# Performance work log

Measured on AMD Instinct MI355X. Metric: run time of the kernel, lower is better.

Reference implementation:

```python
import jax, jax.numpy as jnp
import numpy as np

N, E = 50000, 1600000
F_IN, C1, H, C2, G, NCLS = 256, 16, 4, 32, 64, 10


def setup_inputs() -> dict:
    ks = jax.random.split(jax.random.key(0), 14)
    x = jax.random.normal(ks[0], (N, F_IN), dtype=jnp.float32)
    edge_index = jax.random.randint(ks[1], (2, E), 0, N, dtype=jnp.int32)
    batch = jnp.sort(jax.random.randint(ks[2], (N,), 0, G, dtype=jnp.int32))
    s1 = 1.0 / np.sqrt(F_IN)
    s2 = 1.0 / np.sqrt(H * C1)
    s3 = 1.0 / np.sqrt(C2)
    return {
        "x": x,
        "edge_index": edge_index,
        "batch": batch,
        "W1": jax.random.normal(ks[3], (F_IN, H * C1), jnp.float32) * s1,
        "att_src1": jax.random.normal(ks[4], (H, C1), jnp.float32) * s2,
        "att_dst1": jax.random.normal(ks[5], (H, C1), jnp.float32) * s2,
        "b1": jnp.zeros((H * C1,), jnp.float32),
        "W2": jax.random.normal(ks[6], (H * C1, C2), jnp.float32) * s2,
        "att_src2": jax.random.normal(ks[7], (1, C2), jnp.float32) * s3,
        "att_dst2": jax.random.normal(ks[8], (1, C2), jnp.float32) * s3,
        "b2": jnp.zeros((C2,), jnp.float32),
        "fc_w": jax.random.normal(ks[9], (C2, NCLS), jnp.float32) * s3,
        "fc_b": jnp.zeros((NCLS,), jnp.float32),
    }


def _gat_conv(x, src, dst, W, a_src, a_dst, b, concat):
    # PyG GATConv: linear per head, LeakyReLU(0.2) edge scores,
    # softmax over incoming edges per destination node, weighted scatter-sum.
    n = x.shape[0]
    heads, ch = a_src.shape
    h = (x @ W).reshape(n, heads, ch)                       # [N, H, C]
    a_s = (h * a_src).sum(-1)                               # [N, H]
    a_d = (h * a_dst).sum(-1)                               # [N, H]
    e = jax.nn.leaky_relu(a_s[src] + a_d[dst], 0.2)         # [E', H]
    m = jax.ops.segment_max(e, dst, num_segments=n)         # [N, H]
    w = jnp.exp(e - m[dst])
    den = jax.ops.segment_sum(w, dst, num_segments=n)
    alpha = w / den[dst]                                    # [E', H]
    out = jax.ops.segment_sum(alpha[:, :, None] * h[src], dst, num_segments=n)
    out = out.reshape(n, heads * ch) if concat else out.mean(axis=1)
    return out + b


def reference(x, edge_index, batch, W1, att_src1, att_dst1, b1,
              W2, att_src2, att_dst2, b2, fc_w, fc_b):
    n = x.shape[0]
    loops = jnp.arange(n, dtype=edge_index.dtype)           # add_self_loops=True
    src = jnp.concatenate([edge_index[0], loops])
    dst = jnp.concatenate([edge_index[1], loops])

    h = jax.nn.elu(_gat_conv(x, src, dst, W1, att_src1, att_dst1, b1, True))
    h = jax.nn.elu(_gat_conv(h, src, dst, W2, att_src2, att_dst2, b2, False))

    # global mean pool over graphs
    sums = jax.ops.segment_sum(h, batch, num_segments=G)    # [G, C2]
    cnt = jax.ops.segment_sum(jnp.ones((n,), h.dtype), batch, num_segments=G)
    pooled = sums / jnp.maximum(cnt, 1.0)[:, None]

    logits = pooled @ fc_w + fc_b
    return jax.nn.log_softmax(logits, axis=1)
```

## Files before the change

### kernel.cpp

```cpp
#include <hip/hip_runtime.h>
#include <hip/hip_bf16.h>

#define GV 64
#define NCLSV 10
#define C2V 32
#define CHUNK 256

using short8 = __attribute__((ext_vector_type(8))) short;
using short4v = __attribute__((ext_vector_type(4))) short;
using f32x4 = __attribute__((ext_vector_type(4))) float;

__device__ __forceinline__ float lrelu(float v) { return v > 0.f ? v : 0.2f * v; }
__device__ __forceinline__ float eluf(float v) { return v > 0.f ? v : expf(v) - 1.f; }

__device__ __forceinline__ unsigned short fbf(float f) {
    unsigned u = __float_as_uint(f);
    u += 0x7fff + ((u >> 16) & 1);
    return (unsigned short)(u >> 16);
}
__device__ __forceinline__ float bff(unsigned short h) {
    return __uint_as_float((unsigned)h << 16);
}

__global__ void zero_kernel(int* p, int n) {
    int i = blockIdx.x * blockDim.x + threadIdx.x;
    if (i < n) p[i] = 0;
}

__global__ void wprep_kernel(const float* __restrict__ W1, const float* __restrict__ W2,
                             short* __restrict__ wt, short* __restrict__ wt2) {
    int t = blockIdx.x * blockDim.x + threadIdx.x;
    for (int e = t; e < 16384; e += gridDim.x * blockDim.x) {
        int k = e >> 6, ch = e & 63;
        wt[ch * 256 + k] = (short)fbf(W1[e]);
    }
    for (int e = t; e < 2048; e += gridDim.x * blockDim.x) {
        int k = e >> 5, ch = e & 31;
        wt2[ch * 64 + k] = (short)fbf(W2[e]);
    }
}

__global__ __launch_bounds__(256) void gemm1_mfma_kernel(
    const float* __restrict__ x, const short* __restrict__ wt,
    const float* __restrict__ as_w, const float* __restrict__ ad_w,
    unsigned short* __restrict__ h1lo, unsigned short* __restrict__ h1hi,
    float* __restrict__ as1, float* __restrict__ ad1, int N) {
    __shared__ __align__(16) short xs[32 * 256];
    int b0 = blockIdx.x * 32;
    int tid = threadIdx.x;
    #pragma unroll
    for (int i = 0; i < 8; ++i) {
        int e = (tid + i * 256) * 4;
        int node = e >> 8, k = e & 255;
        float4 v = make_float4(0.f, 0.f, 0.f, 0.f);
        if (b0 + node < N) v = *(const float4*)&x[(size_t)(b0 + node) * 256 + k];
        short4v hv;
        hv[0] = (short)fbf(v.x); hv[1] = (short)fbf(v.y);
        hv[2] = (short)fbf(v.z); hv[3] = (short)fbf(v.w);
        int bo = node * 512 + k * 2;
        int sw = bo ^ ((node & 7) << 4);
        *(short4v*)((char*)xs + sw) = hv;
    }
    __syncthreads();
    int w = tid >> 6, lane = tid & 63;
    int ng = w >> 1, cg = w & 1;
    int g = lane >> 4, q = lane & 15;
    int rowb = ng * 16 + q;
    int kb = g * 8;
    f32x4 acc[2];
    acc[0] = (f32x4){0.f, 0.f, 0.f, 0.f};
    acc[1] = (f32x4){0.f, 0.f, 0.f, 0.f};
    #pragma unroll
    for (int ks = 0; ks < 8; ++ks) {
        int kk = ks * 32 + kb;
        int off = (rowb * 512 + kk * 2) ^ ((rowb & 7) << 4);
        short8 a = *(const short8*)((const char*)xs + off);
        #pragma unroll
        for (int ct = 0; ct < 2; ++ct) {
            int ch = cg * 32 + ct * 16 + q;
            short8 b = *(const short8*)(wt + ch * 256 + kk);
            acc[ct] = __builtin_amdgcn_mfma_f32_16x16x32_bf16(a, b, acc[ct], 0, 0, 0);
        }
    }
    unsigned short* dst = cg ? h1hi : h1lo;
    #pragma unroll
    for (int ct = 0; ct < 2; ++ct) {
        int chi = cg * 32 + ct * 16 + q;
        int ch32 = ct * 16 + q;
        float asw = as_w[chi], adw = ad_w[chi];
        int head = cg * 2 + ct;
        #pragma unroll
        for (int r = 0; r < 4; ++r) {
            int node = b0 + ng * 16 + g * 4 + r;
            float val = acc[ct][r];
            if (node < N) dst[(size_t)node * 32 + ch32] = fbf(val);
            float vs = val * asw, vd = val * adw;
            vs += __shfl_xor(vs, 1); vs += __shfl_xor(vs, 2);
            vs += __shfl_xor(vs, 4); vs += __shfl_xor(vs, 8);
            vd += __shfl_xor(vd, 1); vd += __shfl_xor(vd, 2);
            vd += __shfl_xor(vd, 4); vd += __shfl_xor(vd, 8);
            if (q == 0 && node < N) {
                as1[node * 4 + head] = vs;
                ad1[node * 4 + head] = vd;
            }
        }
    }
}

__global__ __launch_bounds__(256) void bucketPre_kernel(
    const int* __restrict__ ei, int E, int EE, int* __restrict__ bcnt,
    int* __restrict__ pbase) {
    __shared__ int hist[256];
    int span = (EE + gridDim.x - 1) / gridDim.x;
    int s0 = blockIdx.x * span;
    int s1 = min(s0 + span, EE);
    hist[threadIdx.x] = 0;
    __syncthreads();
    for (int i = s0 + threadIdx.x; i < s1; i += 256) {
        int d = (i < E) ? ei[E + i] : i - E;
        atomicAdd(&hist[d >> 8], 1);
    }
    __syncthreads();
    int c = hist[threadIdx.x];
    int base = 0;
    if (c) base = atomicAdd(&bcnt[threadIdx.x], c);
    pbase[blockIdx.x * 256 + threadIdx.x] = base;
}

__global__ void bscan_kernel(const int* __restrict__ bcnt, int* __restrict__ bucketoff,
                             int* __restrict__ rowoff, int N, int EE) {
    __shared__ int wtot[4];
    int v = bcnt[threadIdx.x];
    int lane = threadIdx.x & 63, w = threadIdx.x >> 6;
    int inc = v;
    for (int o = 1; o < 64; o <<= 1) { int t = __shfl_up(inc, o); if (lane >= o) inc += t; }
    if (lane == 63) wtot[w] = inc;
    __syncthreads();
    int woff = 0;
    #pragma unroll
    for (int i = 0; i < 4; ++i) woff += (i < w) ? wtot[i] : 0;
    bucketoff[threadIdx.x + 1] = woff + inc;
    if (threadIdx.x == 0) { bucketoff[0] = 0; rowoff[N] = EE; }
}

__global__ __launch_bounds__(256) void bucketA_kernel(
    const int* __restrict__ ei, int E, int EE,
    const int* __restrict__ bucketoff, const int* __restrict__ pbase,
    int* __restrict__ bbuf) {
    __shared__ int base[256];
    __shared__ int cur[256];
    int span = (EE + gridDim.x - 1) / gridDim.x;
    int s0 = blockIdx.x * span;
    int s1 = min(s0 + span, EE);
    if (s0 >= s1) return;
    base[threadIdx.x] = bucketoff[threadIdx.x] + pbase[blockIdx.x * 256 + threadIdx.x];
    cur[threadIdx.x] = 0;
    __syncthreads();
    for (int i = s0 + threadIdx.x; i < s1; i += 256) {
        int s, d;
        if (i < E) { s = ei[i]; d = ei[E + i]; } else { s = d = i - E; }
        int b = d >> 8;
        int lr = atomicAdd(&cur[b], 1);
        bbuf[base[b] + lr] = ((d & 255) << 24) | s;
    }
}

__global__ __launch_bounds__(256) void bucketB_kernel(
    const int* __restrict__ bucketoff, const int* __restrict__ bbuf,
    int* __restrict__ rowoff, int* __restrict__ ssrc, int N) {
    int k = blockIdx.x;
    __shared__ int cnt[256];
    __shared__ int excl[256];
    __shared__ int cur[256];
    __shared__ int wtot[4];
    cnt[threadIdx.x] = 0; cur[threadIdx.x] = 0;
    __syncthreads();
    int lo = bucketoff[k], hi = bucketoff[k + 1];
    for (int i = lo + threadIdx.x; i < hi; i += 256)
        atomicAdd(&cnt[(bbuf[i] >> 24) & 255], 1);
    __syncthreads();
    int v = cnt[threadIdx.x];
    int lane = threadIdx.x & 63, w = threadIdx.x >> 6;
    int inc = v;
    for (int o = 1; o < 64; o <<= 1) { int t = __shfl_up(inc, o); if (lane >= o) inc += t; }
    if (lane == 63) wtot[w] = inc;
    __syncthreads();
    int woff = 0;
    #pragma unroll
    for (int i = 0; i < 4; ++i) woff += (i < w) ? wtot[i] : 0;
    int e = woff + inc - v;
    excl[threadIdx.x] = e;
    int dst = (k << 8) + threadIdx.x;
    if (dst < N) rowoff[dst] = lo + e;
    __syncthreads();
    for (int i = lo + threadIdx.x; i < hi; i += 256) {
        int pv = bbuf[i];
        int dlow = (pv >> 24) & 255;
        int lr = atomicAdd(&cur[dlow], 1);
        ssrc[lo + excl[dlow] + lr] = pv & 0xFFFFFF;
    }
}

__global__ __launch_bounds__(256) void gat1_kernel(
    const int* __restrict__ rowoff, const int* __restrict__ ssrc,
    const float* __restrict__ as1, const float* __restrict__ ad1,
    const unsigned short* __restrict__ tab, const float* __restrict__ b1,
    unsigned short* __restrict__ h2b, int N, int ho) {
    __shared__ int s_s[4][CHUNK];
    __shared__ float s_w[4][2 * CHUNK];
    int wv = threadIdx.x >> 6;
    int lane = threadIdx.x & 63;
    int row = blockIdx.x * 4 + wv;
    if (row >= N) return;
    int beg = rowoff[row], end = rowoff[row + 1];
    int hp = lane >> 5, j = lane & 31;
    int par = lane >> 2, co = lane & 3;
    int hq = co >> 1;
    float adv = ad1[row * 4 + ho + hp];
    float den = 0.f;
    float a[8];
    #pragma unroll
    for (int i = 0; i < 8; ++i) a[i] = 0.f;
    int* sb = s_s[wv];
    float* wb = s_w[wv];
    for (int cb = beg; cb < end; cb += CHUNK) {
        int clen = min(end - cb, CHUNK);
        for (int t = j; t < clen; t += 32) {
            int s = ssrc[cb + t];
            if (hp == 0) sb[t] = s;
            float w = __expf(lrelu(as1[s * 4 + ho + hp] + adv));
            wb[t * 2 + hp] = w;
            den += w;
        }
        for (int t = par; t < clen; t += 16) {
            int s0 = sb[t];
            float w0 = wb[t * 2 + hq];
            short8 p = *(const short8*)&tab[(size_t)s0 * 32 + 8 * co];
            a[0] += w0 * bff((unsigned short)p[0]);
            a[1] += w0 * bff((unsigned short)p[1]);
            a[2] += w0 * bff((unsigned short)p[2]);
            a[3] += w0 * bff((unsigned short)p[3]);
            a[4] += w0 * bff((unsigned short)p[4]);
            a[5] += w0 * bff((unsigned short)p[5]);
            a[6] += w0 * bff((unsigned short)p[6]);
            a[7] += w0 * bff((unsigned short)p[7]);
        }
    }
    den += __shfl_xor(den, 1);
    den += __shfl_xor(den, 2);
    den += __shfl_xor(den, 4);
    den += __shfl_xor(den, 8);
    den += __shfl_xor(den, 16);
    float dd = __shfl(den, hq << 5);
    #pragma unroll
    for (int i = 0; i < 8; ++i) {
        a[i] += __shfl_xor(a[i], 4);
        a[i] += __shfl_xor(a[i], 8);
        a[i] += __shfl_xor(a[i], 16);
        a[i] += __shfl_xor(a[i], 32);
    }
    if (par == 0) {
        float r = 1.f / dd;
        int cbase = (ho >> 1) * 32 + 8 * co;
        short8 o;
        #pragma unroll
        for (int i = 0; i < 8; ++i)
            o[i] = (short)fbf(eluf(a[i] * r + b1[cbase + i]));
        *(short8*)&h2b[(size_t)row * 64 + cbase] = o;
    }
}

__global__ __launch_bounds__(256) void gemm2_mfma_kernel(
    const unsigned short* __restrict__ h2b, const short* __restrict__ wt2,
    const float* __restrict__ as_w, const float* __restrict__ ad_w,
    unsigned short* __restrict__ t2b, float* __restrict__ as2, float* __restrict__ ad2, int N) {
    __shared__ __align__(16) short xs[64 * 64];
    int b0 = blockIdx.x * 64;
    int tid = threadIdx.x;
    #pragma unroll
    for (int i = 0; i < 2; ++i) {
        int e = (tid + i * 256) * 8;
        int node = e >> 6, k = e & 63;
        short8 v = (short8){0, 0, 0, 0, 0, 0, 0, 0};
        if (b0 + node < N) v = *(const short8*)&h2b[(size_t)(b0 + node) * 64 + k];
        int bo = node * 128 + k * 2;
        int sw = bo ^ ((node & 7) << 4);
        *(short8*)((char*)xs + sw) = v;
    }
    __syncthreads();
    int w = tid >> 6, lane = tid & 63;
    int g = lane >> 4, q = lane & 15;
    int rowb = w * 16 + q;
    int kb = g * 8;
    f32x4 acc[2];
    acc[0] = (f32x4){0.f, 0.f, 0.f, 0.f};
    acc[1] = (f32x4){0.f, 0.f, 0.f, 0.f};
    #pragma unroll
    for (int ks = 0; ks < 2; ++ks) {
        int kk = ks * 32 + kb;
        int off = (rowb * 128 + kk * 2) ^ ((rowb & 7) << 4);
        short8 a = *(const short8*)((const char*)xs + off);
        #pragma unroll
        for (int ct = 0; ct < 2; ++ct) {
            int ch = ct * 16 + q;
            short8 b = *(const short8*)(wt2 + ch * 64 + kk);
            acc[ct] = __builtin_amdgcn_mfma_f32_16x16x32_bf16(a, b, acc[ct], 0, 0, 0);
        }
    }
    float asw0 = as_w[q], adw0 = ad_w[q];
    float asw1 = as_w[16 + q], adw1 = ad_w[16 + q];
    #pragma unroll
    for (int r = 0; r < 4; ++r) {
        int node = b0 + w * 16 + g * 4 + r;
        float v0 = acc[0][r], v1 = acc[1][r];
        if (node < N) {
            t2b[(size_t)node * 32 + q] = fbf(v0);
            t2b[(size_t)node * 32 + 16 + q] = fbf(v1);
        }
        float vs = v0 * asw0 + v1 * asw1;
        float vd = v0 * adw0 + v1 * adw1;
        vs += __shfl_xor(vs, 1); vs += __shfl_xor(vs, 2);
        vs += __shfl_xor(vs, 4); vs += __shfl_xor(vs, 8);
        vd += __shfl_xor(vd, 1); vd += __shfl_xor(vd, 2);
        vd += __shfl_xor(vd, 4); vd += __shfl_xor(vd, 8);
        if (q == 0 && node < N) {
            as2[node] = vs;
            ad2[node] = vd;
        }
    }
}

__global__ __launch_bounds__(256) void gat2_kernel(
    const int* __restrict__ rowoff, const int* __restrict__ ssrc,
    const float* __restrict__ as2, const float* __restrict__ ad2,
    const unsigned short* __restrict__ t2b, const float* __restrict__ b2,
    float* __restrict__ h3, int N) {
    __shared__ int s_s[4][CHUNK];
    __shared__ float s_w[4][CHUNK];
    int wv = threadIdx.x >> 6;
    int lane = threadIdx.x & 63;
    int row = blockIdx.x * 4 + wv;
    if (row >= N) return;
    int beg = rowoff[row], end = rowoff[row + 1];
    int par = lane >> 2, co = lane & 3;
    float adv = ad2[row];
    float den = 0.f;
    float a[8];
    #pragma unroll
    for (int i = 0; i < 8; ++i) a[i] = 0.f;
    int* sb = s_s[wv];
    float* wb = s_w[wv];
    for (int cb = beg; cb < end; cb += CHUNK) {
        int clen = min(end - cb, CHUNK);
        for (int t = lane; t < clen; t += 64) {
            int s = ssrc[cb + t];
            sb[t] = s;
            float w = __expf(lrelu(as2[s] + adv));
            wb[t] = w;
            den += w;
        }
        for (int t = par; t < clen; t += 16) {
            int s0 = sb[t];
            float w0 = wb[t];
            short8 p = *(const short8*)&t2b[(size_t)s0 * 32 + 8 * co];
            a[0] += w0 * bff((unsigned short)p[0]);
            a[1] += w0 * bff((unsigned short)p[1]);
            a[2] += w0 * bff((unsigned short)p[2]);
            a[3] += w0 * bff((unsigned short)p[3]);
            a[4] += w0 * bff((unsigned short)p[4]);
            a[5] += w0 * bff((unsigned short)p[5]);
            a[6] += w0 * bff((unsigned short)p[6]);
            a[7] += w0 * bff((unsigned short)p[7]);
        }
    }
    den += __shfl_xor(den, 1);
    den += __shfl_xor(den, 2);
    den += __shfl_xor(den, 4);
    den += __shfl_xor(den, 8);
    den += __shfl_xor(den, 16);
    den += __shfl_xor(den, 32);
    #pragma unroll
    for (int i = 0; i < 8; ++i) {
        a[i] += __shfl_xor(a[i], 4);
        a[i] += __shfl_xor(a[i], 8);
        a[i] += __shfl_xor(a[i], 16);
        a[i] += __shfl_xor(a[i], 32);
    }
    if (par == 0) {
        float r = 1.f / den;
        float4 o0, o1;
        o0.x = eluf(a[0] * r + b2[8 * co]);
        o0.y = eluf(a[1] * r + b2[8 * co + 1]);
        o0.z = eluf(a[2] * r + b2[8 * co + 2]);
        o0.w = eluf(a[3] * r + b2[8 * co + 3]);
        o1.x = eluf(a[4] * r + b2[8 * co + 4]);
        o1.y = eluf(a[5] * r + b2[8 * co + 5]);
        o1.z = eluf(a[6] * r + b2[8 * co + 6]);
        o1.w = eluf(a[7] * r + b2[8 * co + 7]);
        *(float4*)&h3[(size_t)row * 32 + 8 * co] = o0;
        *(float4*)&h3[(size_t)row * 32 + 8 * co + 4] = o1;
    }
}

__device__ __forceinline__ int lowerb(const int* __restrict__ a, int n, int v) {
    int lo = 0, hi = n;
    while (lo < hi) {
        int mid = (lo + hi) >> 1;
        if (a[mid] < v) lo = mid + 1; else hi = mid;
    }
    return lo;
}

__global__ __launch_bounds__(256) void pool_kernel(
    const float* __restrict__ h3, const int* __restrict__ batch,
    float* __restrict__ pooled, float* __restrict__ cnt, int N) {
    int g = blockIdx.x;
    __shared__ int bounds[2];
    if (threadIdx.x == 0) bounds[0] = lowerb(batch, N, g);
    else if (threadIdx.x == 1) bounds[1] = lowerb(batch, N, g + 1);
    __syncthreads();
    int lo = bounds[0], hi = bounds[1];
    int c = threadIdx.x & 31;
    int grp = threadIdx.x >> 5;
    float s = 0.f;
    for (int n = lo + grp; n < hi; n += 8) s += h3[(size_t)n * 32 + c];
    __shared__ float red[8][33];
    red[grp][c] = s;
    __syncthreads();
    if (grp == 0) {
        float t = 0.f;
        for (int k = 0; k < 8; ++k) t += red[k][c];
        pooled[g * C2V + c] = t;
        if (c == 0) cnt[g] = (float)(hi - lo);
    }
}

__global__ void final_kernel(const float* __restrict__ pooled, const float* __restrict__ cnt,
                             const float* __restrict__ fc_w, const float* __restrict__ fc_b,
                             float* __restrict__ out) {
    int g = threadIdx.x;
    if (g >= GV) return;
    float c = cnt[g];
    c = c > 1.f ? c : 1.f;
    float p[C2V];
    for (int j = 0; j < C2V; ++j) p[j] = pooled[g * C2V + j] / c;
    float l[NCLSV];
    float mx = -1e30f;
    for (int k = 0; k < NCLSV; ++k) {
        float acc = fc_b[k];
        for (int j = 0; j < C2V; ++j) acc += p[j] * fc_w[j * NCLSV + k];
        l[k] = acc;
        mx = fmaxf(mx, acc);
    }
    float s = 0.f;
    for (int k = 0; k < NCLSV; ++k) s += expf(l[k] - mx);
    float lse = mx + logf(s);
    for (int k = 0; k < NCLSV; ++k) out[g * NCLSV + k] = l[k] - lse;
}

extern "C" void kernel_launch(void* const* d_in, const int* in_sizes, int n_in,
                              void* d_out, int out_size, void* d_ws, size_t ws_size,
                              hipStream_t stream) {
    const float* x = (const float*)d_in[0];
    const int* ei = (const int*)d_in[1];
    const int* batch = (const int*)d_in[2];
    const float* W1 = (const float*)d_in[3];
    const float* att_src1 = (const float*)d_in[4];
    const float* att_dst1 = (const float*)d_in[5];
    const float* b1 = (const float*)d_in[6];
    const float* W2 = (const float*)d_in[7];
    const float* att_src2 = (const float*)d_in[8];
    const float* att_dst2 = (const float*)d_in[9];
    const float* b2 = (const float*)d_in[10];
    const float* fc_w = (const float*)d_in[11];
    const float* fc_b = (const float*)d_in[12];
    float* out = (float*)d_out;

    int N = in_sizes[0] / 256;
    int E = in_sizes[1] / 2;
    int EE = E + N;
    int NB = (N + 255) >> 8;

    float* ws = (float*)d_ws;
    size_t off = 0;
    int* bcnt = (int*)(ws + off);      off += 256;
    size_t zTot = off;
    int* pbase = (int*)(ws + off);     off += 1024 * 256;
    int* bucketoff = (int*)(ws + off); off += 257;
    float* pooled = ws + off;          off += (size_t)GV * C2V;
    float* cnt = ws + off;             off += (size_t)GV;
    int* rowoff = (int*)(ws + off);    off += (size_t)N + 1;
    int* bbuf = (int*)(ws + off);      off += (size_t)EE;
    int* ssrc = (int*)(ws + off);      off += (size_t)EE;
    short* wt = (short*)(ws + off);    off += 8192;
    short* wt2 = (short*)(ws + off);   off += 1024;
    unsigned short* h1lo = (unsigned short*)(ws + off); off += (size_t)16 * N;
    unsigned short* h1hi = (unsigned short*)(ws + off); off += (size_t)16 * N;
    float* as1 = ws + off;             off += (size_t)4 * N;
    float* ad1 = ws + off;             off += (size_t)4 * N;
    unsigned short* h2b = (unsigned short*)(ws + off); off += (size_t)32 * N;
    unsigned short* t2b = (unsigned short*)(ws + off); off += (size_t)16 * N;
    float* as2 = ws + off;             off += (size_t)N;
    float* ad2 = ws + off;             off += (size_t)N;
    float* h3 = ws + off;              off += (size_t)32 * N;

    zero_kernel<<<1, 256, 0, stream>>>((int*)ws, (int)zTot);
    wprep_kernel<<<9, 256, 0, stream>>>(W1, W2, wt, wt2);

    gemm1_mfma_kernel<<<(N + 31) / 32, 256, 0, stream>>>(
        x, wt, att_src1, att_dst1, h1lo, h1hi, as1, ad1, N);

    bucketPre_kernel<<<1024, 256, 0, stream>>>(ei, E, EE, bcnt, pbase);
    bscan_kernel<<<1, 256, 0, stream>>>(bcnt, bucketoff, rowoff, N, EE);
    bucketA_kernel<<<1024, 256, 0, stream>>>(ei, E, EE, bucketoff, pbase, bbuf);
    bucketB_kernel<<<NB, 256, 0, stream>>>(bucketoff, bbuf, rowoff, ssrc, N);

    gat1_kernel<<<(N + 3) / 4, 256, 0, stream>>>(rowoff, ssrc, as1, ad1, h1lo, b1, h2b, N, 0);
    gat1_kernel<<<(N + 3) / 4, 256, 0, stream>>>(rowoff, ssrc, as1, ad1, h1hi, b1, h2b, N, 2);

    gemm2_mfma_kernel<<<(N + 63) / 64, 256, 0, stream>>>(
        h2b, wt2, att_src2, att_dst2, t2b, as2, ad2, N);

    gat2_kernel<<<(N + 3) / 4, 256, 0, stream>>>(rowoff, ssrc, as2, ad2, t2b, b2, h3, N);

    pool_kernel<<<GV, 256, 0, stream>>>(h3, batch, pooled, cnt, N);
    final_kernel<<<1, 64, 0, stream>>>(pooled, cnt, fc_w, fc_b, out);
}
```

Before: 246.7 us.

## Precompute layer-1 edge weights in CSR build and merge GAT1 head passes

Moves computation of the layer-1 attention exponentials into the CSR bucket kernel, which writes a 16-byte record per edge holding the source index and four fp16 weights. The two per-head-pair gat1 launches become one kernel over a single 64-channel bf16 feature table, so edges are traversed once instead of twice and no shared-memory staging is needed. gat2 also drops its shared-memory chunk staging and computes weights inline per edge. This adds a 16B-per-edge write and read, and storing the weights in fp16 reduces their precision.

```diff
diff --git a/kernel.cpp b/kernel.cpp
--- a/kernel.cpp
+++ b/kernel.cpp
@@ -4,7 +4,6 @@
 #define GV 64
 #define NCLSV 10
 #define C2V 32
-#define CHUNK 256
 
 using short8 = __attribute__((ext_vector_type(8))) short;
 using short4v = __attribute__((ext_vector_type(4))) short;
@@ -20,6 +19,16 @@
 }
 __device__ __forceinline__ float bff(unsigned short h) {
     return __uint_as_float((unsigned)h << 16);
+}
+__device__ __forceinline__ unsigned f2h(float f) {
+    union { _Float16 h; unsigned short u; } cv;
+    cv.h = (_Float16)f;
+    return (unsigned)cv.u;
+}
+__device__ __forceinline__ float h2f(unsigned short u) {
+    union { unsigned short u; _Float16 h; } cv;
+    cv.u = u;
+    return (float)cv.h;
 }
 
 __global__ void zero_kernel(int* p, int n) {
@@ -43,8 +52,7 @@
 __global__ __launch_bounds__(256) void gemm1_mfma_kernel(
     const float* __restrict__ x, const short* __restrict__ wt,
     const float* __restrict__ as_w, const float* __restrict__ ad_w,
-    unsigned short* __restrict__ h1lo, unsigned short* __restrict__ h1hi,
-    float* __restrict__ as1, float* __restrict__ ad1, int N) {
+    unsigned short* __restrict__ h1b, float* __restrict__ as1, float* __restrict__ ad1, int N) {
     __shared__ __align__(16) short xs[32 * 256];
     int b0 = blockIdx.x * 32;
     int tid = threadIdx.x;
@@ -82,18 +90,16 @@
             acc[ct] = __builtin_amdgcn_mfma_f32_16x16x32_bf16(a, b, acc[ct], 0, 0, 0);
         }
     }
-    unsigned short* dst = cg ? h1hi : h1lo;
     #pragma unroll
     for (int ct = 0; ct < 2; ++ct) {
         int chi = cg * 32 + ct * 16 + q;
-        int ch32 = ct * 16 + q;
         float asw = as_w[chi], adw = ad_w[chi];
         int head = cg * 2 + ct;
         #pragma unroll
         for (int r = 0; r < 4; ++r) {
             int node = b0 + ng * 16 + g * 4 + r;
             float val = acc[ct][r];
-            if (node < N) dst[(size_t)node * 32 + ch32] = fbf(val);
+            if (node < N) h1b[(size_t)node * 64 + chi] = fbf(val);
             float vs = val * asw, vd = val * adw;
             vs += __shfl_xor(vs, 1); vs += __shfl_xor(vs, 2);
             vs += __shfl_xor(vs, 4); vs += __shfl_xor(vs, 8);
@@ -167,7 +173,8 @@
 
 __global__ __launch_bounds__(256) void bucketB_kernel(
     const int* __restrict__ bucketoff, const int* __restrict__ bbuf,
-    int* __restrict__ rowoff, int* __restrict__ ssrc, int N) {
+    const float* __restrict__ as1, const float* __restrict__ ad1,
+    int* __restrict__ rowoff, int* __restrict__ ssrc, int4* __restrict__ wrec, int N) {
     int k = blockIdx.x;
     __shared__ int cnt[256];
     __shared__ int excl[256];
@@ -193,80 +200,76 @@
     int dst = (k << 8) + threadIdx.x;
     if (dst < N) rowoff[dst] = lo + e;
     __syncthreads();
+    int dbase = k << 8;
     for (int i = lo + threadIdx.x; i < hi; i += 256) {
         int pv = bbuf[i];
         int dlow = (pv >> 24) & 255;
+        int s = pv & 0xFFFFFF;
+        int d = dbase + dlow;
         int lr = atomicAdd(&cur[dlow], 1);
-        ssrc[lo + excl[dlow] + lr] = pv & 0xFFFFFF;
+        int pos = lo + excl[dlow] + lr;
+        ssrc[pos] = s;
+        float4 a4 = *(const float4*)&as1[s * 4];
+        float4 d4 = *(const float4*)&ad1[d * 4];
+        float w0 = __expf(lrelu(a4.x + d4.x));
+        float w1 = __expf(lrelu(a4.y + d4.y));
+        float w2 = __expf(lrelu(a4.z + d4.z));
+        float w3 = __expf(lrelu(a4.w + d4.w));
+        int4 rec;
+        rec.x = s;
+        rec.y = (int)(f2h(w0) | (f2h(w1) << 16));
+        rec.z = (int)(f2h(w2) | (f2h(w3) << 16));
+        rec.w = 0;
+        wrec[pos] = rec;
     }
 }
 
 __global__ __launch_bounds__(256) void gat1_kernel(
-    const int* __restrict__ rowoff, const int* __restrict__ ssrc,
-    const float* __restrict__ as1, const float* __restrict__ ad1,
-    const unsigned short* __restrict__ tab, const float* __restrict__ b1,
-    unsigned short* __restrict__ h2b, int N, int ho) {
-    __shared__ int s_s[4][CHUNK];
-    __shared__ float s_w[4][2 * CHUNK];
+    const int* __restrict__ rowoff, const int4* __restrict__ wrec,
+    const unsigned short* __restrict__ h1b, const float* __restrict__ b1,
+    unsigned short* __restrict__ h2b, int N) {
     int wv = threadIdx.x >> 6;
     int lane = threadIdx.x & 63;
     int row = blockIdx.x * 4 + wv;
     if (row >= N) return;
     int beg = rowoff[row], end = rowoff[row + 1];
-    int hp = lane >> 5, j = lane & 31;
-    int par = lane >> 2, co = lane & 3;
-    int hq = co >> 1;
-    float adv = ad1[row * 4 + ho + hp];
+    int par = lane >> 3, co = lane & 7, hq = co >> 1;
     float den = 0.f;
     float a[8];
     #pragma unroll
     for (int i = 0; i < 8; ++i) a[i] = 0.f;
-    int* sb = s_s[wv];
-    float* wb = s_w[wv];
-    for (int cb = beg; cb < end; cb += CHUNK) {
-        int clen = min(end - cb, CHUNK);
-        for (int t = j; t < clen; t += 32) {
-            int s = ssrc[cb + t];
-            if (hp == 0) sb[t] = s;
-            float w = __expf(lrelu(as1[s * 4 + ho + hp] + adv));
-            wb[t * 2 + hp] = w;
-            den += w;
-        }
-        for (int t = par; t < clen; t += 16) {
-            int s0 = sb[t];
-            float w0 = wb[t * 2 + hq];
-            short8 p = *(const short8*)&tab[(size_t)s0 * 32 + 8 * co];
-            a[0] += w0 * bff((unsigned short)p[0]);
-            a[1] += w0 * bff((unsigned short)p[1]);
-            a[2] += w0 * bff((unsigned short)p[2]);
-            a[3] += w0 * bff((unsigned short)p[3]);
-            a[4] += w0 * bff((unsigned short)p[4]);
-            a[5] += w0 * bff((unsigned short)p[5]);
-            a[6] += w0 * bff((unsigned short)p[6]);
-            a[7] += w0 * bff((unsigned short)p[7]);
-        }
-    }
-    den += __shfl_xor(den, 1);
-    den += __shfl_xor(den, 2);
-    den += __shfl_xor(den, 4);
+    for (int t = beg + par; t < end; t += 8) {
+        int4 rec = wrec[t];
+        unsigned wpair = (hq & 2) ? (unsigned)rec.z : (unsigned)rec.y;
+        unsigned wb = (hq & 1) ? (wpair >> 16) : (wpair & 0xFFFFu);
+        float w = h2f((unsigned short)wb);
+        den += w;
+        short8 p = *(const short8*)&h1b[(size_t)rec.x * 64 + 8 * co];
+        a[0] += w * bff((unsigned short)p[0]);
+        a[1] += w * bff((unsigned short)p[1]);
+        a[2] += w * bff((unsigned short)p[2]);
+        a[3] += w * bff((unsigned short)p[3]);
+        a[4] += w * bff((unsigned short)p[4]);
+        a[5] += w * bff((unsigned short)p[5]);
+        a[6] += w * bff((unsigned short)p[6]);
+        a[7] += w * bff((unsigned short)p[7]);
+    }
     den += __shfl_xor(den, 8);
     den += __shfl_xor(den, 16);
-    float dd = __shfl(den, hq << 5);
+    den += __shfl_xor(den, 32);
     #pragma unroll
     for (int i = 0; i < 8; ++i) {
-        a[i] += __shfl_xor(a[i], 4);
         a[i] += __shfl_xor(a[i], 8);
         a[i] += __shfl_xor(a[i], 16);
         a[i] += __shfl_xor(a[i], 32);
     }
     if (par == 0) {
-        float r = 1.f / dd;
-        int cbase = (ho >> 1) * 32 + 8 * co;
+        float r = 1.f / den;
         short8 o;
         #pragma unroll
         for (int i = 0; i < 8; ++i)
-            o[i] = (short)fbf(eluf(a[i] * r + b1[cbase + i]));
-        *(short8*)&h2b[(size_t)row * 64 + cbase] = o;
+            o[i] = (short)fbf(eluf(a[i] * r + b1[8 * co + i]));
+        *(short8*)&h2b[(size_t)row * 64 + 8 * co] = o;
     }
 }
 
@@ -335,8 +338,6 @@
     const float* __restrict__ as2, const float* __restrict__ ad2,
     const unsigned short* __restrict__ t2b, const float* __restrict__ b2,
     float* __restrict__ h3, int N) {
-    __shared__ int s_s[4][CHUNK];
-    __shared__ float s_w[4][CHUNK];
     int wv = threadIdx.x >> 6;
     int lane = threadIdx.x & 63;
     int row = blockIdx.x * 4 + wv;
@@ -348,33 +349,20 @@
     float a[8];
     #pragma unroll
     for (int i = 0; i < 8; ++i) a[i] = 0.f;
-    int* sb = s_s[wv];
-    float* wb = s_w[wv];
-    for (int cb = beg; cb < end; cb += CHUNK) {
-        int clen = min(end - cb, CHUNK);
-        for (int t = lane; t < clen; t += 64) {
-            int s = ssrc[cb + t];
-            sb[t] = s;
-            float w = __expf(lrelu(as2[s] + adv));
-            wb[t] = w;
-            den += w;
-        }
-        for (int t = par; t < clen; t += 16) {
-            int s0 = sb[t];
-            float w0 = wb[t];
-            short8 p = *(const short8*)&t2b[(size_t)s0 * 32 + 8 * co];
-            a[0] += w0 * bff((unsigned short)p[0]);
-            a[1] += w0 * bff((unsigned short)p[1]);
-            a[2] += w0 * bff((unsigned short)p[2]);
-            a[3] += w0 * bff((unsigned short)p[3]);
-            a[4] += w0 * bff((unsigned short)p[4]);
-            a[5] += w0 * bff((unsigned short)p[5]);
-            a[6] += w0 * bff((unsigned short)p[6]);
-            a[7] += w0 * bff((unsigned short)p[7]);
-        }
-    }
-    den += __shfl_xor(den, 1);
-    den += __shfl_xor(den, 2);
+    for (int t = beg + par; t < end; t += 16) {
+        int s0 = ssrc[t];
+        float w = __expf(lrelu(as2[s0] + adv));
+        den += w;
+        short8 p = *(const short8*)&t2b[(size_t)s0 * 32 + 8 * co];
+        a[0] += w * bff((unsigned short)p[0]);
+        a[1] += w * bff((unsigned short)p[1]);
+        a[2] += w * bff((unsigned short)p[2]);
+        a[3] += w * bff((unsigned short)p[3]);
+        a[4] += w * bff((unsigned short)p[4]);
+        a[5] += w * bff((unsigned short)p[5]);
+        a[6] += w * bff((unsigned short)p[6]);
+        a[7] += w * bff((unsigned short)p[7]);
+    }
     den += __shfl_xor(den, 4);
     den += __shfl_xor(den, 8);
     den += __shfl_xor(den, 16);
@@ -492,10 +480,11 @@
     int* rowoff = (int*)(ws + off);    off += (size_t)N + 1;
     int* bbuf = (int*)(ws + off);      off += (size_t)EE;
     int* ssrc = (int*)(ws + off);      off += (size_t)EE;
+    off = (off + 3) & ~(size_t)3;
+    int4* wrec = (int4*)(ws + off);    off += (size_t)4 * EE;
     short* wt = (short*)(ws + off);    off += 8192;
     short* wt2 = (short*)(ws + off);   off += 1024;
-    unsigned short* h1lo = (unsigned short*)(ws + off); off += (size_t)16 * N;
-    unsigned short* h1hi = (unsigned short*)(ws + off); off += (size_t)16 * N;
+    unsigned short* h1b = (unsigned short*)(ws + off); off += (size_t)32 * N;
     float* as1 = ws + off;             off += (size_t)4 * N;
     float* ad1 = ws + off;             off += (size_t)4 * N;
     unsigned short* h2b = (unsigned short*)(ws + off); off += (size_t)32 * N;
@@ -508,15 +497,14 @@
     wprep_kernel<<<9, 256, 0, stream>>>(W1, W2, wt, wt2);
 
     gemm1_mfma_kernel<<<(N + 31) / 32, 256, 0, stream>>>(
-        x, wt, att_src1, att_dst1, h1lo, h1hi, as1, ad1, N);
+        x, wt, att_src1, att_dst1, h1b, as1, ad1, N);
 
     bucketPre_kernel<<<1024, 256, 0, stream>>>(ei, E, EE, bcnt, pbase);
     bscan_kernel<<<1, 256, 0, stream>>>(bcnt, bucketoff, rowoff, N, EE);
     bucketA_kernel<<<1024, 256, 0, stream>>>(ei, E, EE, bucketoff, pbase, bbuf);
-    bucketB_kernel<<<NB, 256, 0, stream>>>(bucketoff, bbuf, rowoff, ssrc, N);
-
-    gat1_kernel<<<(N + 3) / 4, 256, 0, stream>>>(rowoff, ssrc, as1, ad1, h1lo, b1, h2b, N, 0);
-    gat1_kernel<<<(N + 3) / 4, 256, 0, stream>>>(rowoff, ssrc, as1, ad1, h1hi, b1, h2b, N, 2);
+    bucketB_kernel<<<NB, 256, 0, stream>>>(bucketoff, bbuf, as1, ad1, rowoff, ssrc, wrec, N);
+
+    gat1_kernel<<<(N + 3) / 4, 256, 0, stream>>>(rowoff, wrec, h1b, b1, h2b, N);
 
     gemm2_mfma_kernel<<<(N + 63) / 64, 256, 0, stream>>>(
         h2b, wt2, att_src2, att_dst2, t2b, as2, ad2, N);
```

Result: faster. 233.4 us (-5.4%).
